# Kernel tuning notes

Measured on AMD Instinct MI355X. Metric: run time of the kernel, lower is better.

The kernel has to match this reference:

```python
import jax, jax.numpy as jnp
import numpy as np

N, E, G = 30000, 240000, 1500
EMB, NODE_DIM, EDGE_DIM, TASKS = 300, 9, 3, 12
L_ENC, L_RAT = 5, 2
GAMMA, T_CON = 0.4, 0.2


def _w(key, shape, fan_in):
    return jax.random.normal(key, shape, jnp.float32) / np.float32(np.sqrt(fan_in))


def setup_inputs() -> dict:
    key = jax.random.key(0)
    ks = jax.random.split(key, 32)
    inp = {}
    inp['x'] = jax.random.normal(ks[0], (N, NODE_DIM), jnp.float32)
    inp['edge_attr'] = jax.random.normal(ks[1], (E, EDGE_DIM), jnp.float32)
    inp['edge_index'] = jax.random.randint(ks[2], (2, E), 0, N, jnp.int32)
    b = jnp.sort(jax.random.randint(ks[3], (N,), 0, G, jnp.int32))
    inp['batch'] = b.at[0].set(0).at[-1].set(G - 1)
    u = jax.random.uniform(ks[4], (N, 2), jnp.float32, 1e-6, 1.0 - 1e-6)
    inp['gumbel'] = -jnp.log(-jnp.log(u))  # standard Gumbel noise (tau=1)
    inp['perm'] = jax.random.permutation(ks[5], G).astype(jnp.int32)
    inp['W_enc'] = _w(ks[6], (NODE_DIM, EMB), NODE_DIM)
    inp['b_enc'] = jnp.zeros((EMB,), jnp.float32)
    inp['We_g'] = _w(ks[7], (L_ENC, EDGE_DIM, EMB), EDGE_DIM)
    inp['be_g'] = jnp.zeros((L_ENC, EMB), jnp.float32)
    inp['W1_g'] = _w(ks[8], (L_ENC, EMB, 2 * EMB), EMB)
    inp['b1_g'] = jnp.zeros((L_ENC, 2 * EMB), jnp.float32)
    inp['W2_g'] = _w(ks[9], (L_ENC, 2 * EMB, EMB), 2 * EMB)
    inp['b2_g'] = jnp.zeros((L_ENC, EMB), jnp.float32)
    inp['We_r'] = _w(ks[10], (L_RAT, EDGE_DIM, EMB), EDGE_DIM)
    inp['be_r'] = jnp.zeros((L_RAT, EMB), jnp.float32)
    inp['W1_r'] = _w(ks[11], (L_RAT, EMB, 2 * EMB), EMB)
    inp['b1_r'] = jnp.zeros((L_RAT, 2 * EMB), jnp.float32)
    inp['W2_r'] = _w(ks[12], (L_RAT, 2 * EMB, EMB), 2 * EMB)
    inp['b2_r'] = jnp.zeros((L_RAT, EMB), jnp.float32)
    inp['Wg1'] = _w(ks[13], (EMB, 2 * EMB), EMB)
    inp['bg1'] = jnp.zeros((2 * EMB,), jnp.float32)
    inp['Wg2'] = _w(ks[14], (2 * EMB, 2), 2 * EMB)
    inp['bg2'] = jnp.zeros((2,), jnp.float32)
    inp['Wp1'] = _w(ks[15], (EMB, 2 * EMB), EMB)
    inp['bp1'] = jnp.zeros((2 * EMB,), jnp.float32)
    inp['Wp2'] = _w(ks[16], (2 * EMB, TASKS), 2 * EMB)
    inp['bp2'] = jnp.zeros((TASKS,), jnp.float32)
    return inp


def _gin_stack(x, src, dst, edge_attr, We, be, W1, b1, W2, b2):
    # GIN-style message passing with edge features, residual, JK='last'.
    L = We.shape[0]
    for l in range(L):
        e = edge_attr @ We[l] + be[l]                               # [E, EMB]
        msg = jax.nn.relu(x[src] + e)                                # gather [E, EMB]
        agg = jax.ops.segment_sum(msg, dst, num_segments=x.shape[0])  # scatter [N, EMB]
        h = jax.nn.relu((agg + x) @ W1[l] + b1[l]) @ W2[l] + b2[l]
        if l < L - 1:
            h = jax.nn.relu(h)
        x = x + h  # residual
    return x


def _mlp2(h, Wa, ba, Wb, bb):
    # Linear -> (BN=identity in eval) -> ReLU -> (Dropout=identity) -> Linear
    return jax.nn.relu(h @ Wa + ba) @ Wb + bb


def _forward(x, edge_attr, gumbel, W_enc, b_enc, We_g, be_g, W1_g, b1_g, W2_g, b2_g,
             We_r, be_r, W1_r, b1_r, W2_r, b2_r, Wg1, bg1, Wg2, bg2, Wp1, bp1, Wp2, bp2,
             edge_index, batch, perm):
    src, dst = edge_index[0], edge_index[1]
    cnt = jnp.clip(jax.ops.segment_sum(jnp.ones((x.shape[0],), jnp.float32), batch, num_segments=G), 1.0)[:, None]

    def gmean(v):
        return jax.ops.segment_sum(v, batch, num_segments=G) / cnt

    x_feat = x @ W_enc + b_enc                                      # node encoder
    h_node = _gin_stack(x_feat, src, dst, edge_attr, We_g, be_g, W1_g, b1_g, W2_g, b2_g)
    x_rat = _gin_stack(x_feat, src, dst, edge_attr, We_r, be_r, W1_r, b1_r, W2_r, b2_r)

    gate_logits = _mlp2(x_rat, Wg1, bg1, Wg2, bg2)                  # [N, 2]
    gate = jax.nn.softmax(gate_logits + gumbel, axis=-1)[:, 1:2]     # gumbel-softmax (soft), keep last col

    h_r = gmean(gate * h_node)
    h_env = gmean((1.0 - gate) * h_node)
    r_num = jax.ops.segment_sum(gate, batch, num_segments=G) + 1e-8
    env_num = jax.ops.segment_sum(1.0 - gate, batch, num_segments=G) + 1e-8

    pred_rem = _mlp2(h_r, Wp1, bp1, Wp2, bp2)
    loss_reg = jnp.abs(r_num / (r_num + env_num) - GAMMA).mean()

    h_out = gmean(h_node)
    na = jnp.linalg.norm(h_r, axis=1)
    nb = jnp.linalg.norm(h_out, axis=1)
    nc = jnp.linalg.norm(h_env, axis=1)
    sim = jnp.exp((h_r @ h_out.T) / (na[:, None] * nb[None, :] + 1e-8) / T_CON)
    sim_cp = jnp.exp((h_r @ h_env.T) / (na[:, None] * nc[None, :] + 1e-8) / T_CON)
    pos = jnp.diagonal(sim)
    loss_con = -jnp.log(pos / (sim_cp.sum(axis=1) + pos)).mean()

    pred_rep = _mlp2(h_r + h_env[perm], Wp1, bp1, Wp2, bp2)
    return pred_rep, pred_rem, loss_reg, loss_con


def reference(x, edge_attr, gumbel, W_enc, b_enc, We_g, be_g, W1_g, b1_g, W2_g, b2_g,
              We_r, be_r, W1_r, b1_r, W2_r, b2_r, Wg1, bg1, Wg2, bg2, Wp1, bp1, Wp2, bp2,
              edge_index, batch, perm):
    return _forward(x, edge_attr, gumbel, W_enc, b_enc, We_g, be_g, W1_g, b1_g, W2_g, b2_g,
                    We_r, be_r, W1_r, b1_r, W2_r, b2_r, Wg1, bg1, Wg2, bg2, Wp1, bp1, Wp2, bp2,
                    edge_index, batch, perm)
```

## Files before the change

kernel.cpp:

```cpp
#include <hip/hip_runtime.h>
#include <hip/hip_bf16.h>

typedef __hip_bfloat16 bf16;
typedef __attribute__((ext_vector_type(8))) short bf16x8;
typedef __attribute__((ext_vector_type(4))) float f32x4;

#define NN 30000
#define NE 240000
#define NG 1500
#define EMB 300
#define HID 600
#define NTASK 12
#define SEM 320
#define SHID 608
#define CG 75
#define NBLK_SCAN 118

__device__ __forceinline__ float tof(bf16 v){ return __bfloat162float(v); }
__device__ __forceinline__ bf16  tob(float v){ return __float2bfloat16(v); }
__device__ __forceinline__ float b2f(unsigned short u){ return __uint_as_float(((unsigned)u)<<16); }

__global__ __launch_bounds__(256) void k_hist(const int* __restrict__ dst, int* __restrict__ deg){
    int e = blockIdx.x*256 + threadIdx.x;
    if (e < NE) atomicAdd(&deg[dst[e]], 1);
}

__global__ __launch_bounds__(256) void k_scanA(const int* __restrict__ deg, int* __restrict__ bsum){
    __shared__ int red[256];
    int b = blockIdx.x, t = threadIdx.x;
    int i = b*256 + t;
    red[t] = (i < NN) ? deg[i] : 0;
    __syncthreads();
    for (int off=128; off>0; off>>=1){ if (t<off) red[t]+=red[t+off]; __syncthreads(); }
    if (t==0) bsum[b] = red[0];
}

__global__ __launch_bounds__(128) void k_scanB(const int* __restrict__ bsum, int* __restrict__ boff){
    __shared__ int s[128];
    int t = threadIdx.x;
    int v = (t < NBLK_SCAN) ? bsum[t] : 0;
    s[t] = v;
    __syncthreads();
    for (int off=1; off<128; off<<=1){
        int add = (t>=off) ? s[t-off] : 0;
        __syncthreads();
        s[t] += add;
        __syncthreads();
    }
    if (t < NBLK_SCAN) boff[t] = s[t] - v;
}

__global__ __launch_bounds__(256) void k_scanC(const int* __restrict__ deg, const int* __restrict__ boff,
                                               int* __restrict__ indptr, int* __restrict__ cursor){
    __shared__ int s[256];
    int b = blockIdx.x, t = threadIdx.x;
    int i = b*256 + t;
    int v = (i < NN) ? deg[i] : 0;
    s[t] = v;
    __syncthreads();
    for (int off=1; off<256; off<<=1){
        int add = (t>=off) ? s[t-off] : 0;
        __syncthreads();
        s[t] += add;
        __syncthreads();
    }
    int excl = s[t] - v + boff[b];
    if (i < NN){ indptr[i] = excl; cursor[i] = excl; }
    if (i == 0) indptr[NN] = NE;
}

__global__ __launch_bounds__(256) void k_scatter(const int* __restrict__ dst, int* __restrict__ cursor,
                                                 int* __restrict__ eid){
    int e = blockIdx.x*256 + threadIdx.x;
    if (e < NE){ int p = atomicAdd(&cursor[dst[e]], 1); eid[p] = e; }
}

__global__ __launch_bounds__(256) void k_eprep(const int* __restrict__ eid, const int* __restrict__ src,
                                               const float* __restrict__ eattr, float4* __restrict__ epack){
    int k = blockIdx.x*256 + threadIdx.x;
    if (k >= NE) return;
    int e = eid[k];
    float4 p;
    p.x = __int_as_float(src[e]);
    p.y = eattr[e*3]; p.z = eattr[e*3+1]; p.w = eattr[e*3+2];
    epack[k] = p;
}

__global__ __launch_bounds__(256) void k_wprep_all(
        const float* __restrict__ W1_g, const float* __restrict__ W2_g,
        const float* __restrict__ W1_r, const float* __restrict__ W2_r,
        const float* __restrict__ Wg1,  const float* __restrict__ Wp1,
        bf16* __restrict__ wt1g, bf16* __restrict__ wt2g,
        bf16* __restrict__ wt1r, bf16* __restrict__ wt2r,
        bf16* __restrict__ wtg1, bf16* __restrict__ wtp1,
        int* __restrict__ deg, const int* __restrict__ batch, int* __restrict__ gstart,
        const float* __restrict__ x, const float* __restrict__ W_enc,
        const float* __restrict__ b_enc, bf16* __restrict__ xfeat,
        float* __restrict__ glogit){
    __shared__ float t[32][33];
    int z = blockIdx.z;
    if (z >= 18){
        int idx = ((z-18)*361 + blockIdx.y*19 + blockIdx.x)*256 + threadIdx.x;
        if (idx >= NN*EMB) return;
        int n = idx / EMB, c = idx - n*EMB;
        float acc = b_enc[c];
        #pragma unroll
        for (int k=0;k<9;k++) acc += x[n*9+k] * W_enc[k*EMB+c];
        xfeat[(size_t)n*SEM + c] = tob(acc);
        return;
    }
    if (z == 16){
        int i = (blockIdx.y*19 + blockIdx.x)*256 + threadIdx.x;
        if (i < NN){ deg[i] = 0; glogit[2*i] = 0.f; glogit[2*i+1] = 0.f; }
        return;
    }
    if (z == 17){
        int g = (blockIdx.y*19 + blockIdx.x)*256 + threadIdx.x;
        if (g > NG) return;
        if (g == NG){ gstart[NG] = NN; return; }
        int lo=0, hi=NN;
        while (lo<hi){ int mid=(lo+hi)>>1; if (batch[mid] < g) lo=mid+1; else hi=mid; }
        gstart[g] = lo;
        return;
    }
    const float* Ws; bf16* Wd; int K, Kp, N;
    if (z < 5)      { Ws = W1_g + (size_t)z*EMB*HID;      Wd = wt1g + (size_t)z*HID*SEM;      K=EMB; Kp=SEM;  N=HID; }
    else if (z < 10){ int l=z-5;  Ws = W2_g + (size_t)l*HID*EMB; Wd = wt2g + (size_t)l*EMB*SHID; K=HID; Kp=SHID; N=EMB; }
    else if (z < 12){ int l=z-10; Ws = W1_r + (size_t)l*EMB*HID; Wd = wt1r + (size_t)l*HID*SEM;  K=EMB; Kp=SEM;  N=HID; }
    else if (z < 14){ int l=z-12; Ws = W2_r + (size_t)l*HID*EMB; Wd = wt2r + (size_t)l*EMB*SHID; K=HID; Kp=SHID; N=EMB; }
    else if (z ==14){ Ws = Wg1; Wd = wtg1; K=EMB; Kp=SEM; N=HID; }
    else            { Ws = Wp1; Wd = wtp1; K=EMB; Kp=SEM; N=HID; }
    int n0 = blockIdx.x*32, k0 = blockIdx.y*32;
    if (n0 >= N || k0 >= Kp) return;
    int tx = threadIdx.x & 31, ty = threadIdx.x >> 5;
    #pragma unroll
    for (int i=0;i<4;i++){
        int k = k0 + ty + i*8, n = n0 + tx;
        t[ty+i*8][tx] = (k<K && n<N) ? Ws[(size_t)k*N+n] : 0.f;
// ... 228 lines not shown
            int cl = (wn*4+j)*16 + lr;
            float bv = bias[min(n0+cl, N-1)];
            #pragma unroll
            for (int r=0;r<4;r++){
                float v = acc[i][j][r] + bv;
                if (relu_out) v = fmaxf(v, 0.f);
                Ct[(rl+r)*CS + cl] = (short)__bfloat16_as_ushort(tob(v));
            }
        }
    }
    __syncthreads();
    #pragma unroll
    for (int p=0;p<8;p++){
        int rl = p*16 + (tid>>4);
        int cl = (tid&15)*8;
        int row = m0 + rl, col = n0 + cl;
        if (row < M && col < N){
            union { short s8[8]; uint4 v; } u;
            u.v = *(uint4*)&Ct[rl*CS + cl];
            if (R){
                const bf16* rp = &R[(size_t)row*ldc + col];
                #pragma unroll
                for (int e=0;e<8;e++){
                    float v = b2f((unsigned short)u.s8[e]) + tof(rp[e]);
                    u.s8[e] = (short)__bfloat16_as_ushort(tob(v));
                }
            }
            *(uint4*)&C[(size_t)row*ldc + col] = u.v;
        }
    }
}

__global__ __launch_bounds__(256) void k_gemm2(const bf16* __restrict__ A, const bf16* __restrict__ Bt,
        const float* __restrict__ bias, const bf16* __restrict__ R, bf16* __restrict__ C,
        int M, int N, int Kp, int ldc, int relu_out){
    __shared__ __align__(16) char ldsbuf[34816];
    gemm_body(A, Bt, bias, R, C, M, N, Kp, ldc, relu_out, (short*)ldsbuf,
              blockIdx.y*128, blockIdx.x*128);
}

__global__ __launch_bounds__(256) void k_gemm2z(
        const bf16* __restrict__ A0, const bf16* __restrict__ A1,
        const bf16* __restrict__ Bt0, const bf16* __restrict__ Bt1,
        const float* __restrict__ bias0, const float* __restrict__ bias1,
        const bf16* __restrict__ R0, const bf16* __restrict__ R1,
        bf16* __restrict__ C0, bf16* __restrict__ C1,
        int M, int N, int Kp, int ldc, int relu0, int relu1){
    __shared__ __align__(16) char ldsbuf[34816];
    int m0 = blockIdx.y*128, n0 = blockIdx.x*128;
    if (blockIdx.z == 0) gemm_body(A0, Bt0, bias0, R0, C0, M, N, Kp, ldc, relu0, (short*)ldsbuf, m0, n0);
    else                 gemm_body(A1, Bt1, bias1, R1, C1, M, N, Kp, ldc, relu1, (short*)ldsbuf, m0, n0);
}

__device__ __forceinline__ void gemm64_body(const bf16* __restrict__ A, const bf16* __restrict__ Bt,
        const float* __restrict__ bias, const bf16* __restrict__ R, bf16* __restrict__ C,
        int M, int N, int Kp, int ldc, int relu_out, short* lds, int m0, int n0){
    short* Ct = lds;
    const int CS = 72;
    int tid = threadIdx.x;
    int wave = tid >> 6, lane = tid & 63;
    int wm = wave >> 1, wn = wave & 1;

    int srow = tid >> 1;
    int sq   = (tid & 1) * 2;
    int grA = min(m0 + srow, M-1);
    const bf16* pA = A + (size_t)grA*Kp + sq*8;
    int aoff0 = ((srow>>4)*64 +  sq   *16 + (srow&15))*8;
    int aoff1 = ((srow>>4)*64 + (sq+1)*16 + (srow&15))*8;

    int brow = tid >> 2;
    int bq   = tid & 3;
    int grB = min(n0 + brow, N-1);
    const bf16* pB = Bt + (size_t)grB*Kp + bq*8;
    int boff = ((brow>>4)*64 + bq*16 + (brow&15))*8;

    f32x4 acc[4][2];
    #pragma unroll
    for (int i=0;i<4;i++){
        #pragma unroll
        for (int j=0;j<2;j++) acc[i][j] = (f32x4){0.f,0.f,0.f,0.f};
    }

    int KC = Kp >> 5;
    uint4 ra0 = *(const uint4*)(pA);
    uint4 ra1 = *(const uint4*)(pA + 8);
    uint4 rb0 = *(const uint4*)(pB);
    *(uint4*)(lds + aoff0)       = ra0;
    *(uint4*)(lds + aoff1)       = ra1;
    *(uint4*)(lds + 4096 + boff) = rb0;
    __syncthreads();
    if (KC > 1){
        ra0 = *(const uint4*)(pA + 32); ra1 = *(const uint4*)(pA + 40);
        rb0 = *(const uint4*)(pB + 32);
    }

    for (int kc=0; kc<KC; ++kc){
        short* cbuf = lds + (kc & 1)*6144;
        short* nbuf = lds + ((kc+1) & 1)*6144;
        if (kc+1 < KC){
            *(uint4*)(nbuf + aoff0)       = ra0;
            *(uint4*)(nbuf + aoff1)       = ra1;
            *(uint4*)(nbuf + 4096 + boff) = rb0;
            if (kc+2 < KC){
                const bf16* qA = pA + (kc+2)*32;
                ra0 = *(const uint4*)(qA); ra1 = *(const uint4*)(qA+8);
                rb0 = *(const uint4*)(pB + (kc+2)*32);
            }
        }
        bf16x8 af[4], bfr[2];
        #pragma unroll
        for (int i=0;i<4;i++) af[i]  = *(const bf16x8*)(cbuf + ((wm*4+i)*64 + lane)*8);
        #pragma unroll
        for (int j=0;j<2;j++) bfr[j] = *(const bf16x8*)(cbuf + 4096 + ((wn*2+j)*64 + lane)*8);
        #pragma unroll
        for (int i=0;i<4;i++){
            #pragma unroll
            for (int j=0;j<2;j++)
                acc[i][j] = __builtin_amdgcn_mfma_f32_16x16x32_bf16(af[i], bfr[j], acc[i][j], 0, 0, 0);
        }
        __syncthreads();
    }

    int lq = lane >> 4, lr = lane & 15;
    #pragma unroll
    for (int i=0;i<4;i++){
        int rl = (wm*4+i)*16 + lq*4;
        #pragma unroll
        for (int j=0;j<2;j++){
            int cl = (wn*2+j)*16 + lr;
            float bv = bias[min(n0+cl, N-1)];
            #pragma unroll
            for (int r=0;r<4;r++){
                float v = acc[i][j][r] + bv;
                if (relu_out) v = fmaxf(v, 0.f);
                Ct[(rl+r)*CS + cl] = (short)__bfloat16_as_ushort(tob(v));
            }
        }
    }
    __syncthreads();
    #pragma unroll
    for (int p=0;p<4;p++){
        int rl = p*32 + (tid>>3);
        int cl = (tid&7)*8;
        int row = m0 + rl, col = n0 + cl;
        if (row < M && col < N){
            union { short s8[8]; uint4 v; } u;
            u.v = *(uint4*)&Ct[rl*CS + cl];
            if (R){
                const bf16* rp = &R[(size_t)row*ldc + col];
                #pragma unroll
                for (int e=0;e<8;e++){
                    float v = b2f((unsigned short)u.s8[e]) + tof(rp[e]);
                    u.s8[e] = (short)__bfloat16_as_ushort(tob(v));
                }
            }
            *(uint4*)&C[(size_t)row*ldc + col] = u.v;
        }
    }
}

__global__ __launch_bounds__(256) void k_gemm64(const bf16* __restrict__ A, const bf16* __restrict__ Bt,
        const float* __restrict__ bias, const bf16* __restrict__ R, bf16* __restrict__ C,
        int M, int N, int Kp, int ldc, int relu_out){
    __shared__ __align__(16) char ldsbuf[24576];
    gemm64_body(A, Bt, bias, R, C, M, N, Kp, ldc, relu_out, (short*)ldsbuf,
                blockIdx.y*128, blockIdx.x*64);
}

__global__ __launch_bounds__(256) void k_gemm64z(
        const bf16* __restrict__ A0, const bf16* __restrict__ A1,
        const bf16* __restrict__ Bt0, const bf16* __restrict__ Bt1,
        const float* __restrict__ bias0, const float* __restrict__ bias1,
        const bf16* __restrict__ R0, const bf16* __restrict__ R1,
        bf16* __restrict__ C0, bf16* __restrict__ C1,
        int M, int N, int Kp, int ldc, int relu0, int relu1){
    __shared__ __align__(16) char ldsbuf[24576];
    int m0 = blockIdx.y*128, n0 = blockIdx.x*64;
    if (blockIdx.z == 0) gemm64_body(A0, Bt0, bias0, R0, C0, M, N, Kp, ldc, relu0, (short*)ldsbuf, m0, n0);
    else                 gemm64_body(A1, Bt1, bias1, R1, C1, M, N, Kp, ldc, relu1, (short*)ldsbuf, m0, n0);
}

__device__ __forceinline__ void gate_gemm_body(const bf16* __restrict__ A, const bf16* __restrict__ Bt,
        const float* __restrict__ bias, const float* __restrict__ Wg2, float* __restrict__ glogit,
        int M, int N, int Kp, short* lds, int m0, int n0){
    int tid = threadIdx.x;
    int wave = tid >> 6, lane = tid & 63;
    int wm = wave >> 1, wn = wave & 1;

    int srow = tid >> 1;
    int sq   = (tid & 1) * 2;
    int grA = min(m0 + srow, M-1);
    int grB = min(n0 + srow, N-1);
    const bf16* pA = A  + (size_t)grA*Kp + sq*8;
    const bf16* pB = Bt + (size_t)grB*Kp + sq*8;
    int aoff0 = ((srow>>4)*64 +  sq   *16 + (srow&15))*8;
    int aoff1 = ((srow>>4)*64 + (sq+1)*16 + (srow&15))*8;

    f32x4 acc[4][4];
    #pragma unroll
    for (int i=0;i<4;i++){
        #pragma unroll
        for (int j=0;j<4;j++) acc[i][j] = (f32x4){0.f,0.f,0.f,0.f};
    }

    int KC = Kp >> 5;
    uint4 ra0 = *(const uint4*)(pA);
    uint4 ra1 = *(const uint4*)(pA + 8);
    uint4 rb0 = *(const uint4*)(pB);
    uint4 rb1 = *(const uint4*)(pB + 8);
    *(uint4*)(lds + aoff0)        = ra0;
    *(uint4*)(lds + aoff1)        = ra1;
    *(uint4*)(lds + 4096 + aoff0) = rb0;
    *(uint4*)(lds + 4096 + aoff1) = rb1;
    __syncthreads();
    if (KC > 1){
        ra0 = *(const uint4*)(pA + 32); ra1 = *(const uint4*)(pA + 40);
        rb0 = *(const uint4*)(pB + 32); rb1 = *(const uint4*)(pB + 40);
    }

    for (int kc=0; kc<KC; ++kc){
        short* cbuf = lds + (kc & 1)*8192;
        short* nbuf = lds + ((kc+1) & 1)*8192;
        if (kc+1 < KC){
            *(uint4*)(nbuf + aoff0)        = ra0;
            *(uint4*)(nbuf + aoff1)        = ra1;
            *(uint4*)(nbuf + 4096 + aoff0) = rb0;
            *(uint4*)(nbuf + 4096 + aoff1) = rb1;
            if (kc+2 < KC){
                const bf16* qA = pA + (kc+2)*32;
                const bf16* qB = pB + (kc+2)*32;
                ra0 = *(const uint4*)(qA); ra1 = *(const uint4*)(qA+8);
                rb0 = *(const uint4*)(qB); rb1 = *(const uint4*)(qB+8);
// ... 4 lines not shown
        for (int i=0;i<4;i++) af[i]  = *(const bf16x8*)(cbuf + ((wm*4+i)*64 + lane)*8);
        #pragma unroll
        for (int j=0;j<4;j++) bfr[j] = *(const bf16x8*)(cbuf + 4096 + ((wn*4+j)*64 + lane)*8);
        #pragma unroll
        for (int i=0;i<4;i++){
            #pragma unroll
            for (int j=0;j<4;j++)
                acc[i][j] = __builtin_amdgcn_mfma_f32_16x16x32_bf16(af[i], bfr[j], acc[i][j], 0, 0, 0);
        }
        __syncthreads();
    }

    int lq = lane >> 4, lr = lane & 15;
    #pragma unroll
    for (int i=0;i<4;i++){
        #pragma unroll
        for (int r=0;r<4;r++){
            int row = m0 + (wm*4+i)*16 + lq*4 + r;
            float p0 = 0.f, p1 = 0.f;
            #pragma unroll
            for (int j=0;j<4;j++){
                int cl = (wn*4+j)*16 + lr;
                int col = n0 + cl;
                float v = fmaxf(acc[i][j][r] + bias[min(col, N-1)], 0.f);
                if (col < N){ p0 += v * Wg2[col*2]; p1 += v * Wg2[col*2+1]; }
            }
            #pragma unroll
            for (int m=1; m<16; m<<=1){ p0 += __shfl_xor(p0, m); p1 += __shfl_xor(p1, m); }
            if (lr == 0 && row < M){
                atomicAdd(&glogit[row*2],   p0);
                atomicAdd(&glogit[row*2+1], p1);
            }
        }
    }
}

__global__ __launch_bounds__(256) void k_gatepair(
        const bf16* __restrict__ Ag, const bf16* __restrict__ Btg, const float* __restrict__ bg,
        const float* __restrict__ Wg2, float* __restrict__ glogit,
        const bf16* __restrict__ A1, const bf16* __restrict__ Bt1, const float* __restrict__ b1,
        bf16* __restrict__ C1){
    __shared__ __align__(16) char ldsbuf[34816];
    int bid = blockIdx.x;
    if (bid < 1175){
        gate_gemm_body(Ag, Btg, bg, Wg2, glogit, NN, HID, SEM, (short*)ldsbuf,
                       (bid/5)*128, (bid%5)*128);
    } else {
        int gb = bid - 1175;
        gemm_body(A1, Bt1, b1, nullptr, C1, NN, HID, SEM, SHID, 1, (short*)ldsbuf,
                  (gb/5)*128, (gb%5)*128);
    }
}

__global__ __launch_bounds__(256) void k_gatefin(const float* __restrict__ glogit,
        const float* __restrict__ bg2, const float* __restrict__ gumbel, float* __restrict__ gate){
    int i = blockIdx.x*256 + threadIdx.x;
    if (i >= NN) return;
    float l0 = glogit[2*i]   + bg2[0] + gumbel[2*i];
    float l1 = glogit[2*i+1] + bg2[1] + gumbel[2*i+1];
    float m = fmaxf(l0, l1);
    float e0 = expf(l0-m), e1 = expf(l1-m);
    gate[i] = e1/(e0+e1);
}

__device__ __forceinline__ void stage_tile(const short* __restrict__ P, int RB, int K, int r0, int k0,
                                           short (*lds)[64][8], int tid){
    #pragma unroll
    for (int s=0;s<2;s++){
        int seg = tid*2+s;
        int row = seg>>2, q = seg&3;
        int gr = r0 + row;
        int gk = k0 + q*8;
        union { short s8[8]; uint4 v; } u;
        if (gr < RB && gk + 8 <= K){
            const uint2* p = (const uint2*)(P + (size_t)gr*K + gk);
            uint2 lo = p[0], hi = p[1];
            u.v.x = lo.x; u.v.y = lo.y; u.v.z = hi.x; u.v.w = hi.y;
        } else {
            #pragma unroll
            for (int j=0;j<8;j++){
                int kk = gk + j;
                u.s8[j] = (gr < RB && kk < K) ? P[(size_t)gr*K + kk] : (short)0;
            }
        }
        *(uint4*)&lds[row>>4][q*16 + (row&15)][0] = u.v;
    }
}

__device__ __forceinline__ void sim_body(const bf16* __restrict__ A, const bf16* __restrict__ Bt,
                      const float* __restrict__ na, const float* __restrict__ nc, float* __restrict__ S,
                      char* ldsraw){
    short (*Asl)[64][8] = (short(*)[64][8])ldsraw;
    short (*Bsl)[64][8] = (short(*)[64][8])(ldsraw + 8192);
    int tid = threadIdx.x;
    int wave = tid >> 6, lane = tid & 63;
    int wm = wave >> 1, wn = wave & 1;
    int m0 = blockIdx.y*128, n0 = blockIdx.x*128;
    f32x4 acc[4][4];
    #pragma unroll
    for (int i=0;i<4;i++){
        #pragma unroll
        for (int j=0;j<4;j++) acc[i][j] = (f32x4){0.f,0.f,0.f,0.f};
    }
    for (int k0=0; k0<SEM; k0+=32){
        stage_tile((const short*)A,  NG, SEM, m0, k0, Asl, tid);
        stage_tile((const short*)Bt, NG, SEM, n0, k0, Bsl, tid);
        __syncthreads();
        bf16x8 af[4], bfr[4];
        #pragma unroll
        for (int i=0;i<4;i++) af[i]  = *(const bf16x8*)&Asl[wm*4+i][lane][0];
        #pragma unroll
        for (int j=0;j<4;j++) bfr[j] = *(const bf16x8*)&Bsl[wn*4+j][lane][0];
        #pragma unroll
        for (int i=0;i<4;i++){
            #pragma unroll
            for (int j=0;j<4;j++)
                acc[i][j] = __builtin_amdgcn_mfma_f32_16x16x32_bf16(af[i], bfr[j], acc[i][j], 0, 0, 0);
        }
        __syncthreads();
    }
    int lq = lane >> 4, lr = lane & 15;
    #pragma unroll
    for (int i=0;i<4;i++){
        #pragma unroll
        for (int r=0;r<4;r++){
            int row = m0 + (wm*4+i)*16 + lq*4 + r;
            float nar = na[min(row, NG-1)];
            float rsum = 0.f;
            #pragma unroll
            for (int j=0;j<4;j++){
                int col = n0 + (wn*4+j)*16 + lr;
                float ncj = nc[min(col, NG-1)];
                float e = expf(acc[i][j][r] * 5.0f / (nar*ncj + 1e-8f));
                if (row < NG && col < NG) rsum += e;
            }
            #pragma unroll
            for (int m=1; m<16; m<<=1) rsum += __shfl_xor(rsum, m);
            if (lr == 0 && row < NG) atomicAdd(&S[row], rsum);
        }
    }
}

__global__ __launch_bounds__(256) void k_simhead(const bf16* __restrict__ hrb, const bf16* __restrict__ henvb,
        const float* __restrict__ na, const float* __restrict__ nc, float* __restrict__ Ssum,
        const bf16* __restrict__ Pbuf, const bf16* __restrict__ wtp1, const float* __restrict__ bp1,
        bf16* __restrict__ hidP){
    __shared__ __align__(16) char ldsbuf[34816];
    if (blockIdx.z == 0){
        if (blockIdx.x >= 12 || blockIdx.y >= 12) return;
        sim_body(hrb, henvb, na, nc, Ssum, ldsbuf);
    } else {
        if (blockIdx.x >= 5) return;
        gemm_body(Pbuf, wtp1, bp1, nullptr, hidP, 2*NG, HID, SEM, SHID, 1, (short*)ldsbuf,
                  blockIdx.y*128, blockIdx.x*128);
    }
}

__global__ __launch_bounds__(320) void k_pool(const bf16* __restrict__ h, const float* __restrict__ gate,
                      const int* __restrict__ gstart, float* __restrict__ sumh, float* __restrict__ sumgh,
                      float* __restrict__ rnum, float* __restrict__ cntf){
    int g = blockIdx.x, c = threadIdx.x;
    if (c >= EMB) return;
    int n0 = gstart[g], n1 = gstart[g+1];
    float sh=0.f, sg=0.f, sgate=0.f;
    for (int n=n0;n<n1;n++){
        float v = tof(h[(size_t)n*SEM+c]);
        float gt = gate[n];
        sh += v; sg += gt*v;
        if (c==0) sgate += gt;
    }
    sumh[g*EMB+c] = sh; sumgh[g*EMB+c] = sg;
    if (c==0){ rnum[g] = sgate; cntf[g] = (float)(n1-n0); }
}

__global__ __launch_bounds__(320) void k_meannorm(const float* __restrict__ sumh, const float* __restrict__ sumgh,
                      const float* __restrict__ cntf, float* __restrict__ hr, float* __restrict__ henv,
                      float* __restrict__ hout, bf16* __restrict__ hrb, bf16* __restrict__ henvb,
                      bf16* __restrict__ P, float* __restrict__ na, float* __restrict__ nc,
                      float* __restrict__ pos, float* __restrict__ Ssum){
    int g = blockIdx.x, c = threadIdx.x;
    float r=0.f, e=0.f, o=0.f;
    int idx = g*SEM + c;
    if (c < EMB){
        int off = g*EMB + c;
        float inv = 1.f / fmaxf(cntf[g], 1.f);
        float sh = sumh[off], sg = sumgh[off];
        r = sg*inv; e = (sh-sg)*inv; o = sh*inv;
        hr[off] = r; henv[off] = e; hout[off] = o;
        hrb[idx] = tob(r); henvb[idx] = tob(e); P[idx] = tob(r);
    } else {
        hrb[idx] = tob(0.f); henvb[idx] = tob(0.f); P[idx] = tob(0.f);
        if (c == 319) Ssum[g] = 0.f;
    }
    float srr=r*r, soo=o*o, see=e*e, sro=r*o;
    #pragma unroll
    for (int off=32; off>0; off>>=1){
        srr += __shfl_down(srr,off); soo += __shfl_down(soo,off);
        see += __shfl_down(see,off); sro += __shfl_down(sro,off);
    }
    __shared__ float ws[4][5];
    int wv = c >> 6, ln = c & 63;
    if (ln == 0){ ws[0][wv]=srr; ws[1][wv]=soo; ws[2][wv]=see; ws[3][wv]=sro; }
    __syncthreads();
    if (c == 0){
        float a=0.f,b=0.f,c2=0.f,d=0.f;
        #pragma unroll
        for (int i=0;i<5;i++){ a+=ws[0][i]; b+=ws[1][i]; c2+=ws[2][i]; d+=ws[3][i]; }
        float sa = sqrtf(a), sb = sqrtf(b), sc = sqrtf(c2);
        na[g] = sa; nc[g] = sc;
        pos[g] = expf(d/(sa*sb + 1e-8f) * 5.0f);
    }
}

__global__ __launch_bounds__(256) void k_pbuild2(const float* __restrict__ hr, const float* __restrict__ henv,
                      const int* __restrict__ perm, bf16* __restrict__ P){
    int idx = blockIdx.x*256 + threadIdx.x;
    if (idx >= NG*SEM) return;
    int g = idx / SEM, c = idx - g*SEM;
    P[(size_t)(NG+g)*SEM + c] = (c < EMB)
        ? tob(hr[g*EMB+c] + henv[(size_t)perm[g]*EMB + c])
        : tob(0.f);
}

__global__ __launch_bounds__(256) void k_pred(const bf16* __restrict__ hidP, const float* __restrict__ Wp2,
                      const float* __restrict__ bp2, float* __restrict__ out){
    int r = blockIdx.x*4 + (threadIdx.x >> 6);
    int lane = threadIdx.x & 63;
    if (r >= 2*NG) return;
    float acc[NTASK];
    #pragma unroll
    for (int t=0;t<NTASK;t++) acc[t] = 0.f;
    for (int i=lane;i<HID;i+=64){
        float h = tof(hidP[(size_t)r*SHID+i]);
        const float4* wp = (const float4*)&Wp2[i*NTASK];
        float4 wa = wp[0], wb = wp[1], wc = wp[2];
        acc[0]+=h*wa.x; acc[1]+=h*wa.y; acc[2]+=h*wa.z; acc[3]+=h*wa.w;
        acc[4]+=h*wb.x; acc[5]+=h*wb.y; acc[6]+=h*wb.z; acc[7]+=h*wb.w;
        acc[8]+=h*wc.x; acc[9]+=h*wc.y; acc[10]+=h*wc.z; acc[11]+=h*wc.w;
    }
    #pragma unroll
    for (int t=0;t<NTASK;t++){
        for (int off=32; off>0; off>>=1) acc[t] += __shfl_down(acc[t], off);
// ... 33 lines not shown
    const int*   eidx   = (const int*)d_in[2];
    const int*   batch  = (const int*)d_in[3];
    const float* gumbel = (const float*)d_in[4];
    const int*   perm   = (const int*)d_in[5];
    const float* W_enc  = (const float*)d_in[6];
    const float* b_enc  = (const float*)d_in[7];
    const float* We_g   = (const float*)d_in[8];
    const float* be_g   = (const float*)d_in[9];
    const float* W1_g   = (const float*)d_in[10];
    const float* b1_g   = (const float*)d_in[11];
    const float* W2_g   = (const float*)d_in[12];
    const float* b2_g   = (const float*)d_in[13];
    const float* We_r   = (const float*)d_in[14];
    const float* be_r   = (const float*)d_in[15];
    const float* W1_r   = (const float*)d_in[16];
    const float* b1_r   = (const float*)d_in[17];
    const float* W2_r   = (const float*)d_in[18];
    const float* b2_r   = (const float*)d_in[19];
    const float* Wg1    = (const float*)d_in[20];
    const float* bg1    = (const float*)d_in[21];
    const float* Wg2    = (const float*)d_in[22];
    const float* bg2    = (const float*)d_in[23];
    const float* Wp1    = (const float*)d_in[24];
    const float* bp1    = (const float*)d_in[25];
    const float* Wp2    = (const float*)d_in[26];
    const float* bp2    = (const float*)d_in[27];
    float* out = (float*)d_out;

    const int* srcArr = eidx;
    const int* dstArr = eidx + NE;

    char* w = (char*)d_ws;
    size_t off = 0;
    auto alloc = [&](size_t bytes)->char*{ char* p = w + off; off += (bytes + 255) & ~(size_t)255; return p; };
    bf16* xfeat = (bf16*)alloc((size_t)NN*SEM*2);
    bf16* cur_r = (bf16*)alloc((size_t)NN*SEM*2);
    bf16* cur_g = (bf16*)alloc((size_t)NN*SEM*2);
    bf16* apx   = (bf16*)alloc((size_t)NN*SEM*2);
    bf16* apx2  = (bf16*)alloc((size_t)NN*SEM*2);
    char* midc  = alloc((size_t)NN*SHID*2);
    bf16* mid_r = (bf16*)midc;
    bf16* Pbuf   = (bf16*)(midc + 12*1024*1024);
    bf16* hidP   = (bf16*)(midc + 20*1024*1024);
    bf16* mid_g = (bf16*)alloc((size_t)NN*SHID*2);
    bf16* wt1g  = (bf16*)alloc((size_t)5*HID*SEM*2);
    bf16* wt2g  = (bf16*)alloc((size_t)5*EMB*SHID*2);
    bf16* wt1r  = (bf16*)alloc((size_t)2*HID*SEM*2);
    bf16* wt2r  = (bf16*)alloc((size_t)2*EMB*SHID*2);
    bf16* wtg1  = (bf16*)alloc((size_t)HID*SEM*2);
    bf16* wtp1  = (bf16*)alloc((size_t)HID*SEM*2);
    float4* epack = (float4*)alloc((size_t)NE*16);
    float* gate  = (float*)alloc((size_t)NN*4);
    float* glogit= (float*)alloc((size_t)NN*2*4);
    float* sumh  = (float*)alloc((size_t)NG*EMB*4);
    float* sumgh = (float*)alloc((size_t)NG*EMB*4);
    float* hr    = (float*)alloc((size_t)NG*EMB*4);
    float* henv  = (float*)alloc((size_t)NG*EMB*4);
    float* hout  = (float*)alloc((size_t)NG*EMB*4);
    bf16* hrb    = (bf16*)alloc((size_t)NG*SEM*2);
    bf16* henvb  = (bf16*)alloc((size_t)NG*SEM*2);
    float* rnum  = (float*)alloc(NG*4);
    float* cntf  = (float*)alloc(NG*4);
    float* na    = (float*)alloc(NG*4);
    float* ncv   = (float*)alloc(NG*4);
    float* pos   = (float*)alloc(NG*4);
    float* Ssum  = (float*)alloc(NG*4);
    int* deg     = (int*)alloc((size_t)NN*4);
    int* indptr  = (int*)alloc((size_t)(NN+1)*4);
    int* cursor  = (int*)alloc((size_t)NN*4);
    int* eid     = (int*)alloc((size_t)NE*4);
    int* gstart  = (int*)alloc((size_t)(NG+1)*4);
    int* bsum    = (int*)alloc((size_t)NBLK_SCAN*4);
    int* boff    = (int*)alloc((size_t)NBLK_SCAN*4);

    const int NB_NE  = (NE+255)/256;
    const int NB_AG  = (NN*CG+255)/256;
    const int NB_GP  = (NG*SEM+255)/256;

    dim3 gwp(19, 19, 18 + 98);
    k_wprep_all<<<gwp, 256, 0, stream>>>(W1_g, W2_g, W1_r, W2_r, Wg1, Wp1,
                                         wt1g, wt2g, wt1r, wt2r, wtg1, wtp1,
                                         deg, batch, gstart, x, W_enc, b_enc, xfeat, glogit);

    k_hist   <<<NB_NE, 256, 0, stream>>>(dstArr, deg);
    k_scanA  <<<NBLK_SCAN, 256, 0, stream>>>(deg, bsum);
    k_scanB  <<<1, 128, 0, stream>>>(bsum, boff);
    k_scanC  <<<NBLK_SCAN, 256, 0, stream>>>(deg, boff, indptr, cursor);
    k_scatter<<<NB_NE, 256, 0, stream>>>(dstArr, cursor, eid);
    k_eprep  <<<NB_NE, 256, 0, stream>>>(eid, srcArr, eattr, epack);

    dim3 gm1z((HID+127)/128, (NN+127)/128, 2);
    dim3 gm64z((EMB+63)/64, (NN+127)/128, 2);
    dim3 gm1((HID+127)/128, (NN+127)/128);
    dim3 gm64((EMB+63)/64, (NN+127)/128);
    dim3 gagz(NB_AG, 1, 2);

    k_agg4d<<<NB_AG, 256, 0, stream>>>(xfeat, We_r, be_r, We_g, be_g, epack, indptr, apx, apx2);
    k_gemm2z<<<gm1z, 256, 0, stream>>>(apx, apx2, wt1r, wt1g, b1_r, b1_g,
                                       nullptr, nullptr, mid_r, mid_g, NN, HID, SEM, SHID, 1, 1);
    k_gemm64z<<<gm64z, 256, 0, stream>>>(mid_r, mid_g, wt2r, wt2g, b2_r, b2_g,
                                         xfeat, xfeat, cur_r, cur_g, NN, EMB, SHID, SEM, 1, 1);

    k_agg4z<<<gagz, 256, 0, stream>>>(cur_r, cur_g, We_r + 3*EMB, We_g + 3*EMB, be_r + EMB, be_g + EMB,
                                      epack, indptr, apx, apx2);
    k_gemm2z<<<gm1z, 256, 0, stream>>>(apx, apx2, wt1r + (size_t)HID*SEM, wt1g + (size_t)HID*SEM,
                                       b1_r + HID, b1_g + HID, nullptr, nullptr, mid_r, mid_g,
                                       NN, HID, SEM, SHID, 1, 1);
    k_gemm64z<<<gm64z, 256, 0, stream>>>(mid_r, mid_g, wt2r + (size_t)EMB*SHID, wt2g + (size_t)EMB*SHID,
                                         b2_r + EMB, b2_g + EMB, cur_r, cur_g, cur_r, cur_g,
                                         NN, EMB, SHID, SEM, 0, 1);

    k_agg4 <<<NB_AG, 256, 0, stream>>>(cur_g, We_g + 2*3*EMB, be_g + 2*EMB, epack, indptr, apx2);
    k_gatepair<<<2350, 256, 0, stream>>>(cur_r, wtg1, bg1, Wg2, glogit,
                                         apx2, wt1g + (size_t)2*HID*SEM, b1_g + 2*HID, mid_g);
    k_gatefin<<<(NN+255)/256, 256, 0, stream>>>(glogit, bg2, gumbel, gate);
    k_gemm64<<<gm64, 256, 0, stream>>>(mid_g, wt2g + (size_t)2*EMB*SHID, b2_g + 2*EMB, cur_g, cur_g,
                                       NN, EMB, SHID, SEM, 1);

    for (int l=3; l<5; l++){
        k_agg4 <<<NB_AG, 256, 0, stream>>>(cur_g, We_g + l*3*EMB, be_g + l*EMB, epack, indptr, apx2);
        k_gemm2<<<gm1, 256, 0, stream>>>(apx2, wt1g + (size_t)l*HID*SEM, b1_g + l*HID, nullptr, mid_g,
                                         NN, HID, SEM, SHID, 1);
        k_gemm64<<<gm64, 256, 0, stream>>>(mid_g, wt2g + (size_t)l*EMB*SHID, b2_g + l*EMB, cur_g, cur_g,
                                           NN, EMB, SHID, SEM, (l<4)?1:0);
    }

    k_pool    <<<NG, 320, 0, stream>>>(cur_g, gate, gstart, sumh, sumgh, rnum, cntf);
    k_meannorm<<<NG, 320, 0, stream>>>(sumh, sumgh, cntf, hr, henv, hout, hrb, henvb, Pbuf,
                                       na, ncv, pos, Ssum);
    k_pbuild2 <<<NB_GP, 256, 0, stream>>>(hr, henv, perm, Pbuf);
    dim3 gsh(12, 24, 2);
    k_simhead<<<gsh, 256, 0, stream>>>(hrb, henvb, na, ncv, Ssum, Pbuf, wtp1, bp1, hidP);
    k_pred  <<<(2*NG+3)/4, 256, 0, stream>>>(hidP, Wp2, bp2, out);
    k_loss  <<<1, 256, 0, stream>>>(cntf, rnum, pos, Ssum, out);
}
```

Baseline: 1.005 ms.

## Widen second GIN GEMM tile to 160 columns and fuse small kernels

The second MLP GEMM (K=608, N=300) now uses a 128x160 tile instead of 128x64, so two column blocks cover the 300 outputs. This cuts redundant A-tile reloads from five blocks to two. The gate softmax is folded into the layer-2 GEMM launch as extra blocks, pooling and mean/norm are merged into one kernel, and edge scatter and packing are fused. The wider tile uses more accumulators and LDS per block, which may lower occupancy, and it wastes some columns on the second block's padding.

Measured after the change: 911.8 us. -9.2%, faster.

```diff
diff --git a/kernel.cpp b/kernel.cpp
--- a/kernel.cpp
+++ b/kernel.cpp
@@ -69,21 +69,15 @@
     if (i == 0) indptr[NN] = NE;
 }
 
-__global__ __launch_bounds__(256) void k_scatter(const int* __restrict__ dst, int* __restrict__ cursor,
-                                                 int* __restrict__ eid){
+__global__ __launch_bounds__(256) void k_scatterprep(const int* __restrict__ dst, const int* __restrict__ src,
+                      const float* __restrict__ eattr, int* __restrict__ cursor, float4* __restrict__ epack){
     int e = blockIdx.x*256 + threadIdx.x;
-    if (e < NE){ int p = atomicAdd(&cursor[dst[e]], 1); eid[p] = e; }
-}
-
-__global__ __launch_bounds__(256) void k_eprep(const int* __restrict__ eid, const int* __restrict__ src,
-                                               const float* __restrict__ eattr, float4* __restrict__ epack){
-    int k = blockIdx.x*256 + threadIdx.x;
-    if (k >= NE) return;
-    int e = eid[k];
-    float4 p;
-    p.x = __int_as_float(src[e]);
-    p.y = eattr[e*3]; p.z = eattr[e*3+1]; p.w = eattr[e*3+2];
-    epack[k] = p;
+    if (e >= NE) return;
+    int p = atomicAdd(&cursor[dst[e]], 1);
+    float4 q;
+    q.x = __int_as_float(src[e]);
+    q.y = eattr[e*3]; q.z = eattr[e*3+1]; q.w = eattr[e*3+2];
+    epack[p] = q;
 }
 
 __global__ __launch_bounds__(256) void k_wprep_all(
@@ -418,11 +412,12 @@
     else                 gemm_body(A1, Bt1, bias1, R1, C1, M, N, Kp, ldc, relu1, (short*)ldsbuf, m0, n0);
 }
 
-__device__ __forceinline__ void gemm64_body(const bf16* __restrict__ A, const bf16* __restrict__ Bt,
+__device__ __forceinline__ void gemm160_body(const bf16* __restrict__ A, const bf16* __restrict__ Bt,
         const float* __restrict__ bias, const bf16* __restrict__ R, bf16* __restrict__ C,
         int M, int N, int Kp, int ldc, int relu_out, short* lds, int m0, int n0){
     short* Ct = lds;
-    const int CS = 72;
+    const int CS = 168;
+    const int BUF = 9216;
     int tid = threadIdx.x;
     int wave = tid >> 6, lane = tid & 63;
     int wm = wave >> 1, wn = wave & 1;
@@ -434,54 +429,70 @@
     int aoff0 = ((srow>>4)*64 +  sq   *16 + (srow&15))*8;
     int aoff1 = ((srow>>4)*64 + (sq+1)*16 + (srow&15))*8;
 
-    int brow = tid >> 2;
-    int bq   = tid & 3;
-    int grB = min(n0 + brow, N-1);
-    const bf16* pB = Bt + (size_t)grB*Kp + bq*8;
-    int boff = ((brow>>4)*64 + bq*16 + (brow&15))*8;
-
-    f32x4 acc[4][2];
+    int cB0 = tid, cB1 = tid + 256, cB2 = tid + 512;
+    int br0 = cB0>>2, bq0 = cB0&3;
+    int br1 = cB1>>2, bq1 = cB1&3;
+    int br2 = cB2>>2, bq2 = cB2&3;
+    const bf16* pB0 = Bt + (size_t)min(n0+br0, N-1)*Kp + bq0*8;
+    const bf16* pB1 = Bt + (size_t)min(n0+br1, N-1)*Kp + bq1*8;
+    const bf16* pB2 = Bt + (size_t)min(n0+br2, N-1)*Kp + bq2*8;
+    int boff0 = 4096 + ((br0>>4)*64 + bq0*16 + (br0&15))*8;
+    int boff1 = 4096 + ((br1>>4)*64 + bq1*16 + (br1&15))*8;
+    int boff2 = 4096 + ((br2>>4)*64 + bq2*16 + (br2&15))*8;
+    bool b3 = (tid < 128);
+
+    f32x4 acc[4][5];
     #pragma unroll
     for (int i=0;i<4;i++){
         #pragma unroll
-        for (int j=0;j<2;j++) acc[i][j] = (f32x4){0.f,0.f,0.f,0.f};
+        for (int j=0;j<5;j++) acc[i][j] = (f32x4){0.f,0.f,0.f,0.f};
     }
 
     int KC = Kp >> 5;
     uint4 ra0 = *(const uint4*)(pA);
     uint4 ra1 = *(const uint4*)(pA + 8);
-    uint4 rb0 = *(const uint4*)(pB);
-    *(uint4*)(lds + aoff0)       = ra0;
-    *(uint4*)(lds + aoff1)       = ra1;
-    *(uint4*)(lds + 4096 + boff) = rb0;
+    uint4 rb0 = *(const uint4*)(pB0);
+    uint4 rb1 = *(const uint4*)(pB1);
+    uint4 rb2 = {0,0,0,0};
+    if (b3) rb2 = *(const uint4*)(pB2);
+    *(uint4*)(lds + aoff0) = ra0;
+    *(uint4*)(lds + aoff1) = ra1;
+    *(uint4*)(lds + boff0) = rb0;
+    *(uint4*)(lds + boff1) = rb1;
+    if (b3) *(uint4*)(lds + boff2) = rb2;
     __syncthreads();
     if (KC > 1){
-        ra0 = *(const uint4*)(pA + 32); ra1 = *(const uint4*)(pA + 40);
-        rb0 = *(const uint4*)(pB + 32);
+        ra0 = *(const uint4*)(pA + 32);  ra1 = *(const uint4*)(pA + 40);
+        rb0 = *(const uint4*)(pB0 + 32); rb1 = *(const uint4*)(pB1 + 32);
+        if (b3) rb2 = *(const uint4*)(pB2 + 32);
     }
 
     for (int kc=0; kc<KC; ++kc){
-        short* cbuf = lds + (kc & 1)*6144;
-        short* nbuf = lds + ((kc+1) & 1)*6144;
+        short* cbuf = lds + (kc & 1)*BUF;
+        short* nbuf = lds + ((kc+1) & 1)*BUF;
         if (kc+1 < KC){
-            *(uint4*)(nbuf + aoff0)       = ra0;
-            *(uint4*)(nbuf + aoff1)       = ra1;
-            *(uint4*)(nbuf + 4096 + boff) = rb0;
+            *(uint4*)(nbuf + aoff0) = ra0;
+            *(uint4*)(nbuf + aoff1) = ra1;
+            *(uint4*)(nbuf + boff0) = rb0;
+            *(uint4*)(nbuf + boff1) = rb1;
+            if (b3) *(uint4*)(nbuf + boff2) = rb2;
             if (kc+2 < KC){
                 const bf16* qA = pA + (kc+2)*32;
                 ra0 = *(const uint4*)(qA); ra1 = *(const uint4*)(qA+8);
-                rb0 = *(const uint4*)(pB + (kc+2)*32);
+                rb0 = *(const uint4*)(pB0 + (kc+2)*32);
+                rb1 = *(const uint4*)(pB1 + (kc+2)*32);
+                if (b3) rb2 = *(const uint4*)(pB2 + (kc+2)*32);
             }
         }
-        bf16x8 af[4], bfr[2];
+        bf16x8 af[4], bfr[5];
         #pragma unroll
         for (int i=0;i<4;i++) af[i]  = *(const bf16x8*)(cbuf + ((wm*4+i)*64 + lane)*8);
         #pragma unroll
-        for (int j=0;j<2;j++) bfr[j] = *(const bf16x8*)(cbuf + 4096 + ((wn*2+j)*64 + lane)*8);
+        for (int j=0;j<5;j++) bfr[j] = *(const bf16x8*)(cbuf + 4096 + ((wn*5+j)*64 + lane)*8);
         #pragma unroll
         for (int i=0;i<4;i++){
             #pragma unroll
-            for (int j=0;j<2;j++)
+            for (int j=0;j<5;j++)
                 acc[i][j] = __builtin_amdgcn_mfma_f32_16x16x32_bf16(af[i], bfr[j], acc[i][j], 0, 0, 0);
         }
         __syncthreads();
@@ -492,8 +503,8 @@
     for (int i=0;i<4;i++){
         int rl = (wm*4+i)*16 + lq*4;
         #pragma unroll
-        for (int j=0;j<2;j++){
-            int cl = (wn*2+j)*16 + lr;
+        for (int j=0;j<5;j++){
+            int cl = (wn*5+j)*16 + lr;
             float bv = bias[min(n0+cl, N-1)];
             #pragma unroll
             for (int r=0;r<4;r++){
@@ -505,45 +516,66 @@
     }
     __syncthreads();
     #pragma unroll
-    for (int p=0;p<4;p++){
-        int rl = p*32 + (tid>>3);
-        int cl = (tid&7)*8;
-        int row = m0 + rl, col = n0 + cl;
-        if (row < M && col < N){
+    for (int p=0;p<10;p++){
+        int c = p*256 + tid;
+        int row = c / 20, colc = c - (c/20)*20;
+        int grow = m0 + row, gcol = n0 + colc*8;
+        if (grow < M && gcol < N){
             union { short s8[8]; uint4 v; } u;
-            u.v = *(uint4*)&Ct[rl*CS + cl];
+            u.v = *(uint4*)&Ct[row*CS + colc*8];
             if (R){
-                const bf16* rp = &R[(size_t)row*ldc + col];
+                const bf16* rp = &R[(size_t)grow*ldc + gcol];
                 #pragma unroll
                 for (int e=0;e<8;e++){
                     float v = b2f((unsigned short)u.s8[e]) + tof(rp[e]);
                     u.s8[e] = (short)__bfloat16_as_ushort(tob(v));
                 }
             }
-            *(uint4*)&C[(size_t)row*ldc + col] = u.v;
-        }
-    }
-}
-
-__global__ __launch_bounds__(256) void k_gemm64(const bf16* __restrict__ A, const bf16* __restrict__ Bt,
+            *(uint4*)&C[(size_t)grow*ldc + gcol] = u.v;
+        }
+    }
+}
+
+__global__ __launch_bounds__(256) void k_gemm160(const bf16* __restrict__ A, const bf16* __restrict__ Bt,
         const float* __restrict__ bias, const bf16* __restrict__ R, bf16* __restrict__ C,
         int M, int N, int Kp, int ldc, int relu_out){
-    __shared__ __align__(16) char ldsbuf[24576];
-    gemm64_body(A, Bt, bias, R, C, M, N, Kp, ldc, relu_out, (short*)ldsbuf,
-                blockIdx.y*128, blockIdx.x*64);
-}
-
-__global__ __launch_bounds__(256) void k_gemm64z(
+    __shared__ __align__(16) char ldsbuf[43008];
+    gemm160_body(A, Bt, bias, R, C, M, N, Kp, ldc, relu_out, (short*)ldsbuf,
+                 blockIdx.y*128, blockIdx.x*160);
+}
+
+__global__ __launch_bounds__(256) void k_gemm160z(
         const bf16* __restrict__ A0, const bf16* __restrict__ A1,
         const bf16* __restrict__ Bt0, const bf16* __restrict__ Bt1,
         const float* __restrict__ bias0, const float* __restrict__ bias1,
         const bf16* __restrict__ R0, const bf16* __restrict__ R1,
         bf16* __restrict__ C0, bf16* __restrict__ C1,
         int M, int N, int Kp, int ldc, int relu0, int relu1){
-    __shared__ __align__(16) char ldsbuf[24576];
-    int m0 = blockIdx.y*128, n0 = blockIdx.x*64;
-    if (blockIdx.z == 0) gemm64_body(A0, Bt0, bias0, R0, C0, M, N, Kp, ldc, relu0, (short*)ldsbuf, m0, n0);
-    else                 gemm64_body(A1, Bt1, bias1, R1, C1, M, N, Kp, ldc, relu1, (short*)ldsbuf, m0, n0);
+    __shared__ __align__(16) char ldsbuf[43008];
+    int m0 = blockIdx.y*128, n0 = blockIdx.x*160;
+    if (blockIdx.z == 0) gemm160_body(A0, Bt0, bias0, R0, C0, M, N, Kp, ldc, relu0, (short*)ldsbuf, m0, n0);
+    else                 gemm160_body(A1, Bt1, bias1, R1, C1, M, N, Kp, ldc, relu1, (short*)ldsbuf, m0, n0);
+}
+
+__global__ __launch_bounds__(256) void k_g160gate(
+        const bf16* __restrict__ A, const bf16* __restrict__ Bt, const float* __restrict__ bias,
+        const bf16* __restrict__ R, bf16* __restrict__ C,
+        const float* __restrict__ glogit, const float* __restrict__ bg2,
+        const float* __restrict__ gumbel, float* __restrict__ gate){
+    __shared__ __align__(16) char ldsbuf[43008];
+    int bid = blockIdx.x;
+    if (bid < 470){
+        gemm160_body(A, Bt, bias, R, C, NN, EMB, SHID, SEM, 1, (short*)ldsbuf,
+                     (bid>>1)*128, (bid&1)*160);
+    } else {
+        int i = (bid-470)*256 + threadIdx.x;
+        if (i >= NN) return;
+        float l0 = glogit[2*i]   + bg2[0] + gumbel[2*i];
+        float l1 = glogit[2*i+1] + bg2[1] + gumbel[2*i+1];
+        float m = fmaxf(l0, l1);
+        float e0 = expf(l0-m), e1 = expf(l1-m);
+        gate[i] = e1/(e0+e1);
+    }
 }
 
 __device__ __forceinline__ void gate_gemm_body(const bf16* __restrict__ A, const bf16* __restrict__ Bt,
@@ -654,17 +686,6 @@
     }
 }
 
-__global__ __launch_bounds__(256) void k_gatefin(const float* __restrict__ glogit,
-        const float* __restrict__ bg2, const float* __restrict__ gumbel, float* __restrict__ gate){
-    int i = blockIdx.x*256 + threadIdx.x;
-    if (i >= NN) return;
-    float l0 = glogit[2*i]   + bg2[0] + gumbel[2*i];
-    float l1 = glogit[2*i+1] + bg2[1] + gumbel[2*i+1];
-    float m = fmaxf(l0, l1);
-    float e0 = expf(l0-m), e1 = expf(l1-m);
-    gate[i] = e1/(e0+e1);
-}
-
 __device__ __forceinline__ void stage_tile(const short* __restrict__ P, int RB, int K, int r0, int k0,
                                            short (*lds)[64][8], int tid){
     #pragma unroll
@@ -758,38 +779,32 @@
     }
 }
 
-__global__ __launch_bounds__(320) void k_pool(const bf16* __restrict__ h, const float* __restrict__ gate,
-                      const int* __restrict__ gstart, float* __restrict__ sumh, float* __restrict__ sumgh,
-                      float* __restrict__ rnum, float* __restrict__ cntf){
+__global__ __launch_bounds__(320) void k_poolmean(const bf16* __restrict__ h, const float* __restrict__ gate,
+                      const int* __restrict__ gstart, float* __restrict__ hr, float* __restrict__ henv,
+                      bf16* __restrict__ hrb, bf16* __restrict__ henvb, bf16* __restrict__ P,
+                      float* __restrict__ na, float* __restrict__ nc, float* __restrict__ pos,
+                      float* __restrict__ rnum, float* __restrict__ cntf, float* __restrict__ Ssum){
     int g = blockIdx.x, c = threadIdx.x;
-    if (c >= EMB) return;
     int n0 = gstart[g], n1 = gstart[g+1];
     float sh=0.f, sg=0.f, sgate=0.f;
-    for (int n=n0;n<n1;n++){
-        float v = tof(h[(size_t)n*SEM+c]);
-        float gt = gate[n];
-        sh += v; sg += gt*v;
-        if (c==0) sgate += gt;
-    }
-    sumh[g*EMB+c] = sh; sumgh[g*EMB+c] = sg;
-    if (c==0){ rnum[g] = sgate; cntf[g] = (float)(n1-n0); }
-}
-
-__global__ __launch_bounds__(320) void k_meannorm(const float* __restrict__ sumh, const float* __restrict__ sumgh,
-                      const float* __restrict__ cntf, float* __restrict__ hr, float* __restrict__ henv,
-                      float* __restrict__ hout, bf16* __restrict__ hrb, bf16* __restrict__ henvb,
-                      bf16* __restrict__ P, float* __restrict__ na, float* __restrict__ nc,
-                      float* __restrict__ pos, float* __restrict__ Ssum){
-    int g = blockIdx.x, c = threadIdx.x;
+    if (c < EMB){
+        for (int n=n0;n<n1;n++){
+            float v = tof(h[(size_t)n*SEM+c]);
+            float gt = gate[n];
+            sh += v; sg += gt*v;
+            if (c==0) sgate += gt;
+        }
+    }
+    float cnt = (float)(n1-n0);
+    float inv = 1.f / fmaxf(cnt, 1.f);
     float r=0.f, e=0.f, o=0.f;
     int idx = g*SEM + c;
     if (c < EMB){
         int off = g*EMB + c;
-        float inv = 1.f / fmaxf(cntf[g], 1.f);
-        float sh = sumh[off], sg = sumgh[off];
         r = sg*inv; e = (sh-sg)*inv; o = sh*inv;
-        hr[off] = r; henv[off] = e; hout[off] = o;
+        hr[off] = r; henv[off] = e;
         hrb[idx] = tob(r); henvb[idx] = tob(e); P[idx] = tob(r);
+        if (c==0){ rnum[g] = sgate; cntf[g] = cnt; }
     } else {
         hrb[idx] = tob(0.f); henvb[idx] = tob(0.f); P[idx] = tob(0.f);
         if (c == 319) Ssum[g] = 0.f;
@@ -929,11 +944,8 @@
     float4* epack = (float4*)alloc((size_t)NE*16);
     float* gate  = (float*)alloc((size_t)NN*4);
     float* glogit= (float*)alloc((size_t)NN*2*4);
-    float* sumh  = (float*)alloc((size_t)NG*EMB*4);
-    float* sumgh = (float*)alloc((size_t)NG*EMB*4);
     float* hr    = (float*)alloc((size_t)NG*EMB*4);
     float* henv  = (float*)alloc((size_t)NG*EMB*4);
-    float* hout  = (float*)alloc((size_t)NG*EMB*4);
     bf16* hrb    = (bf16*)alloc((size_t)NG*SEM*2);
     bf16* henvb  = (bf16*)alloc((size_t)NG*SEM*2);
     float* rnum  = (float*)alloc(NG*4);
@@ -945,7 +957,6 @@
     int* deg     = (int*)alloc((size_t)NN*4);
     int* indptr  = (int*)alloc((size_t)(NN+1)*4);
     int* cursor  = (int*)alloc((size_t)NN*4);
-    int* eid     = (int*)alloc((size_t)NE*4);
     int* gstart  = (int*)alloc((size_t)(NG+1)*4);
     int* bsum    = (int*)alloc((size_t)NBLK_SCAN*4);
     int* boff    = (int*)alloc((size_t)NBLK_SCAN*4);
@@ -959,52 +970,49 @@
                                          wt1g, wt2g, wt1r, wt2r, wtg1, wtp1,
                                          deg, batch, gstart, x, W_enc, b_enc, xfeat, glogit);
 
-    k_hist   <<<NB_NE, 256, 0, stream>>>(dstArr, deg);
-    k_scanA  <<<NBLK_SCAN, 256, 0, stream>>>(deg, bsum);
-    k_scanB  <<<1, 128, 0, stream>>>(bsum, boff);
-    k_scanC  <<<NBLK_SCAN, 256, 0, stream>>>(deg, boff, indptr, cursor);
-    k_scatter<<<NB_NE, 256, 0, stream>>>(dstArr, cursor, eid);
-    k_eprep  <<<NB_NE, 256, 0, stream>>>(eid, srcArr, eattr, epack);
+    k_hist       <<<NB_NE, 256, 0, stream>>>(dstArr, deg);
+    k_scanA      <<<NBLK_SCAN, 256, 0, stream>>>(deg, bsum);
+    k_scanB      <<<1, 128, 0, stream>>>(bsum, boff);
+    k_scanC      <<<NBLK_SCAN, 256, 0, stream>>>(deg, boff, indptr, cursor);
+    k_scatterprep<<<NB_NE, 256, 0, stream>>>(dstArr, srcArr, eattr, cursor, epack);
 
     dim3 gm1z((HID+127)/128, (NN+127)/128, 2);
-    dim3 gm64z((EMB+63)/64, (NN+127)/128, 2);
+    dim3 gm160z(2, (NN+127)/128, 2);
     dim3 gm1((HID+127)/128, (NN+127)/128);
-    dim3 gm64((EMB+63)/64, (NN+127)/128);
+    dim3 gm160(2, (NN+127)/128);
     dim3 gagz(NB_AG, 1, 2);
 
     k_agg4d<<<NB_AG, 256, 0, stream>>>(xfeat, We_r, be_r, We_g, be_g, epack, indptr, apx, apx2);
     k_gemm2z<<<gm1z, 256, 0, stream>>>(apx, apx2, wt1r, wt1g, b1_r, b1_g,
                                        nullptr, nullptr, mid_r, mid_g, NN, HID, SEM, SHID, 1, 1);
-    k_gemm64z<<<gm64z, 256, 0, stream>>>(mid_r, mid_g, wt2r, wt2g, b2_r, b2_g,
-                                         xfeat, xfeat, cur_r, cur_g, NN, EMB, SHID, SEM, 1, 1);
+    k_gemm160z<<<gm160z, 256, 0, stream>>>(mid_r, mid_g, wt2r, wt2g, b2_r, b2_g,
+                                           xfeat, xfeat, cur_r, cur_g, NN, EMB, SHID, SEM, 1, 1);
 
     k_agg4z<<<gagz, 256, 0, stream>>>(cur_r, cur_g, We_r + 3*EMB, We_g + 3*EMB, be_r + EMB, be_g + EMB,
                                       epack, indptr, apx, apx2);
     k_gemm2z<<<gm1z, 256, 0, stream>>>(apx, apx2, wt1r + (size_t)HID*SEM, wt1g + (size_t)HID*SEM,
                                        b1_r + HID, b1_g + HID, nullptr, nullptr, mid_r, mid_g,
                                        NN, HID, SEM, SHID, 1, 1);
-    k_gemm64z<<<gm64z, 256, 0, stream>>>(mid_r, mid_g, wt2r + (size_t)EMB*SHID, wt2g + (size_t)EMB*SHID,
-                                         b2_r + EMB, b2_g + EMB, cur_r, cur_g, cur_r, cur_g,
-                                         NN, EMB, SHID, SEM, 0, 1);
+    k_gemm160z<<<gm160z, 256, 0, stream>>>(mid_r, mid_g, wt2r + (size_t)EMB*SHID, wt2g + (size_t)EMB*SHID,
+                                           b2_r + EMB, b2_g + EMB, cur_r, cur_g, cur_r, cur_g,
+                                           NN, EMB, SHID, SEM, 0, 1);
 
     k_agg4 <<<NB_AG, 256, 0, stream>>>(cur_g, We_g + 2*3*EMB, be_g + 2*EMB, epack, indptr, apx2);
     k_gatepair<<<2350, 256, 0, stream>>>(cur_r, wtg1, bg1, Wg2, glogit,
                                          apx2, wt1g + (size_t)2*HID*SEM, b1_g + 2*HID, mid_g);
-    k_gatefin<<<(NN+255)/256, 256, 0, stream>>>(glogit, bg2, gumbel, gate);
-    k_gemm64<<<gm64, 256, 0, stream>>>(mid_g, wt2g + (size_t)2*EMB*SHID, b2_g + 2*EMB, cur_g, cur_g,
-                                       NN, EMB, SHID, SEM, 1);
+    k_g160gate<<<588, 256, 0, stream>>>(mid_g, wt2g + (size_t)2*EMB*SHID, b2_g + 2*EMB, cur_g, cur_g,
+                                        glogit, bg2, gumbel, gate);
 
     for (int l=3; l<5; l++){
         k_agg4 <<<NB_AG, 256, 0, stream>>>(cur_g, We_g + l*3*EMB, be_g + l*EMB, epack, indptr, apx2);
         k_gemm2<<<gm1, 256, 0, stream>>>(apx2, wt1g + (size_t)l*HID*SEM, b1_g + l*HID, nullptr, mid_g,
                                          NN, HID, SEM, SHID, 1);
-        k_gemm64<<<gm64, 256, 0, stream>>>(mid_g, wt2g + (size_t)l*EMB*SHID, b2_g + l*EMB, cur_g, cur_g,
-                                           NN, EMB, SHID, SEM, (l<4)?1:0);
-    }
-
-    k_pool    <<<NG, 320, 0, stream>>>(cur_g, gate, gstart, sumh, sumgh, rnum, cntf);
-    k_meannorm<<<NG, 320, 0, stream>>>(sumh, sumgh, cntf, hr, henv, hout, hrb, henvb, Pbuf,
-                                       na, ncv, pos, Ssum);
+        k_gemm160<<<gm160, 256, 0, stream>>>(mid_g, wt2g + (size_t)l*EMB*SHID, b2_g + l*EMB, cur_g, cur_g,
+                                             NN, EMB, SHID, SEM, (l<4)?1:0);
+    }
+
+    k_poolmean<<<NG, 320, 0, stream>>>(cur_g, gate, gstart, hr, henv, hrb, henvb, Pbuf,
+                                       na, ncv, pos, rnum, cntf, Ssum);
     k_pbuild2 <<<NB_GP, 256, 0, stream>>>(hr, henv, perm, Pbuf);
     dim3 gsh(12, 24, 2);
     k_simhead<<<gsh, 256, 0, stream>>>(hrb, henvb, na, ncv, Ssum, Pbuf, wtp1, bp1, hidP);
```
